# Kernel optimization log

Measured on AMD Instinct MI355X. Metric: run time of the kernel, lower is better.

Reference implementation:

```python
import jax, jax.numpy as jnp
import numpy as np

I3 = jnp.eye(3, dtype=jnp.float32)
G_VEC = jnp.array([0.0, 0.0, -9.80665], dtype=jnp.float32)
# Q diag: [cov_omega x3, cov_acc x3, cov_b_omega x3, cov_b_acc x3, cov_Rot_c_i x3, cov_t_c_i x3]
Q_DIAG = jnp.array([1e-3] * 3 + [1e-2] * 3 + [6e-9] * 3 + [2e-4] * 3 + [1e-9] * 3 + [1e-9] * 3, dtype=jnp.float32)
N_NORM_ROT = 100
N_NORM_ROT_CI = 1000


def skew(v):
    z = jnp.zeros_like(v[0])
    return jnp.stack([jnp.stack([z, -v[2], v[1]]),
                      jnp.stack([v[2], z, -v[0]]),
                      jnp.stack([-v[1], v[0], z])])


def so3exp(phi):
    a2 = jnp.sum(phi * phi)
    small = a2 < 1e-12
    a = jnp.sqrt(jnp.where(small, 1.0, a2))
    axis = phi / a
    c, s = jnp.cos(a), jnp.sin(a)
    big = c * I3 + (1.0 - c) * jnp.outer(axis, axis) + s * skew(axis)
    return jnp.where(small, I3 + skew(phi), big)


def sen3exp(xi):
    # SE_2(3) exponential: xi[:3]=rotation, xi[3:9]=(v, p) parts
    phi = xi[:3]
    a2 = jnp.sum(phi * phi)
    small = a2 < 1e-12
    a = jnp.sqrt(jnp.where(small, 1.0, a2))
    axis = phi / a
    c, s = jnp.cos(a), jnp.sin(a)
    sk = skew(axis)
    R = jnp.where(small, I3 + skew(phi),
                  c * I3 + (1.0 - c) * jnp.outer(axis, axis) + s * sk)
    J = jnp.where(small, I3 + 0.5 * skew(phi),
                  (s / a) * I3 + (1.0 - s / a) * jnp.outer(axis, axis) + ((1.0 - c) / a) * sk)
    x = J @ xi[3:].reshape(2, 3).T  # (3,2): columns are dv, dp
    return R, x


def normalize_rot(R):
    # Polar-factor re-orthonormalization (equivalent to the SVD-based
    # normalize_rot for near-rotation matrices), via Newton-Schulz iteration
    # which is smooth and jit/vjp friendly.
    def body(X, _):
        return 1.5 * X - 0.5 * (X @ X.T @ X), None
    X, _ = jax.lax.scan(body, R, None, length=8)
    return X


def from_rpy(roll, pitch, yaw):
    cr, sr = jnp.cos(roll), jnp.sin(roll)
    cp, sp = jnp.cos(pitch), jnp.sin(pitch)
    cy, sy = jnp.cos(yaw), jnp.sin(yaw)
    one = jnp.ones_like(cr)
    zero = jnp.zeros_like(cr)
    Rx = jnp.stack([jnp.stack([one, zero, zero]), jnp.stack([zero, cr, -sr]), jnp.stack([zero, sr, cr])])
    Ry = jnp.stack([jnp.stack([cp, zero, sp]), jnp.stack([zero, one, zero]), jnp.stack([-sp, zero, cp])])
    Rz = jnp.stack([jnp.stack([cy, -sy, zero]), jnp.stack([sy, cy, zero]), jnp.stack([zero, zero, one])])
    return Rz @ Ry @ Rx


def init_covariance():
    P = jnp.zeros((21, 21), dtype=jnp.float32)
    P = P.at[:2, :2].set(1e-3 * jnp.eye(2))     # cov_Rot0 (no yaw error)
    P = P.at[3:5, 3:5].set(0.1 * jnp.eye(2))    # cov_v0
    P = P.at[9:12, 9:12].set(6e-3 * I3)         # cov_b_omega0
    P = P.at[12:15, 12:15].set(4e-3 * I3)       # cov_b_acc0
    P = P.at[15:18, 15:18].set(1e-6 * I3)       # cov_Rot_c_i0
    P = P.at[18:21, 18:21].set(5e-3 * I3)       # cov_t_c_i0
    return P


def propagate_cov(P, Rot, v, p, dt):
    F = jnp.zeros((21, 21), dtype=P.dtype)
    F = F.at[3:6, :3].set(skew(G_VEC))
    F = F.at[6:9, 3:6].set(I3)
    F = F.at[:3, 9:12].set(-Rot)
    F = F.at[3:6, 9:12].set(-skew(v) @ Rot)
    F = F.at[3:6, 12:15].set(-Rot)
    F = F.at[6:9, 9:12].set(-skew(p) @ Rot)
    G = jnp.zeros((21, 18), dtype=P.dtype)
    G = G.at[:3, :3].set(Rot)
    G = G.at[3:6, 3:6].set(Rot)
    G = G.at[9:12, 6:9].set(I3)
    G = G.at[12:15, 9:12].set(I3)
    G = G.at[15:18, 12:15].set(I3)
    G = G.at[18:21, 15:18].set(I3)
    F = F * dt
    G = G * dt
    F2 = F @ F
    Phi = jnp.eye(21, dtype=P.dtype) + F + 0.5 * F2 + (F2 @ F) / 6.0  # 3rd-order expm
    return Phi @ (P + (G * Q_DIAG[None, :]) @ G.T) @ Phi.T


def _step(carry, xs):
    Rot, v, p, b_om, b_ac, Rci, tci, P = carry
    u_i, dt_i, mcov_i, i = xs
    # ---- propagate ----
    acc = Rot @ (u_i[3:6] - b_ac) + G_VEC
    v_n = v + acc * dt_i
    p_n = p + v * dt_i + 0.5 * acc * dt_i * dt_i
    Rot_n = Rot @ so3exp((u_i[:3] - b_om) * dt_i)
    P_n = propagate_cov(P, Rot, v, p, dt_i)
    # ---- update: zero lateral/vertical body-velocity pseudo-measurement ----
    omega = u_i[:3] - b_om
    Rot_body = Rot_n @ Rci
    v_imu = Rot_n.T @ v_n
    v_body = Rci.T @ v_imu + skew(tci) @ omega
    H = jnp.zeros((2, 21), dtype=P.dtype)
    H = H.at[:, 3:6].set(Rot_body.T[1:])
    H = H.at[:, 15:18].set((Rci.T @ skew(v_imu))[1:])
    H = H.at[:, 9:12].set(skew(tci)[1:])
    H = H.at[:, 18:21].set(-skew(omega)[1:])
    r = -v_body[1:]
    Rm = jnp.diag(mcov_i)
    S = H @ P_n @ H.T + Rm                    # (2,2)
    K = jnp.linalg.solve(S, H @ P_n).T        # K = P H^T S^-1 (P, S symmetric)
    dx = K @ r                                 # (21,)
    dR, dxi = sen3exp(dx[:9])
    Rot_u = dR @ Rot_n
    v_u = dR @ v_n + dxi[:, 0]
    p_u = dR @ p_n + dxi[:, 1]
    b_om_u = b_om + dx[9:12]
    b_ac_u = b_ac + dx[12:15]
    Rci_u = so3exp(dx[15:18]) @ Rci
    tci_u = tci + dx[18:21]
    IKH = jnp.eye(21, dtype=P.dtype) - K @ H
    P_u = IKH @ P_n @ IKH.T + K @ Rm @ K.T    # Joseph form
    P_u = 0.5 * (P_u + P_u.T)
    Rot_u = jnp.where(i % N_NORM_ROT == 0, normalize_rot(Rot_u), Rot_u)
    Rci_u = jnp.where(i % N_NORM_ROT_CI == 0, normalize_rot(Rci_u), Rci_u)
    carry = (Rot_u, v_u, p_u, b_om_u, b_ac_u, Rci_u, tci_u, P_u)
    return carry, (Rot_u, v_u, p_u, b_om_u, b_ac_u, Rci_u, tci_u)


def _forward(t, u, measurements_covs, v_mes, p_mes, ang0, N):
    dt = t[1:N] - t[:N - 1]
    Rot0 = from_rpy(ang0[0], ang0[1], ang0[2])
    z3 = jnp.zeros(3, dtype=u.dtype)
    carry0 = (Rot0, v_mes[0], z3, z3, z3, I3, z3, init_covariance())
    xs = (u[1:N], dt, measurements_covs[1:N], jnp.arange(1, N))
    _, ys = jax.lax.scan(_step, carry0, xs)
    Rot = jnp.concatenate([Rot0[None], ys[0]], axis=0)
    v = jnp.concatenate([v_mes[0][None], ys[1]], axis=0)
    p = jnp.concatenate([z3[None], ys[2]], axis=0)
    b_omega = jnp.concatenate([z3[None], ys[3]], axis=0)
    b_acc = jnp.concatenate([z3[None], ys[4]], axis=0)
    Rot_c_i = jnp.concatenate([I3[None], ys[5]], axis=0)
    t_c_i = jnp.concatenate([z3[None], ys[6]], axis=0)
    return (Rot, v, p, b_omega, b_acc, Rot_c_i, t_c_i)


def setup_inputs() -> dict:
    key = jax.random.key(0)
    N = 20000  # 200 s at 100 Hz IMU
    k0, k1, k2, k3, k4, k5 = jax.random.split(key, 6)
    t = jnp.arange(N, dtype=jnp.float32) * 0.01
    gyro = 0.01 * jax.random.normal(k0, (N, 3), dtype=jnp.float32)
    acc = jnp.array([0.0, 0.0, 9.80665], jnp.float32) + 0.1 * jax.random.normal(k1, (N, 3), dtype=jnp.float32)
    u = jnp.concatenate([gyro, acc], axis=1)
    measurements_covs = 0.1 + jax.random.uniform(k2, (N, 2), dtype=jnp.float32)
    v_mes = jax.random.normal(k3, (N, 3), dtype=jnp.float32)
    p_mes = jax.random.normal(k4, (N, 3), dtype=jnp.float32)
    ang0 = 0.01 * jax.random.normal(k5, (3,), dtype=jnp.float32)
    return dict(t=t, u=u, measurements_covs=measurements_covs, v_mes=v_mes, p_mes=p_mes, ang0=ang0, N=N)


def reference(t, u, measurements_covs, v_mes, p_mes, ang0, N):
    return _forward(t, u, measurements_covs, v_mes, p_mes, ang0, N)
```

## Files before the change

### kernel.cpp

```cpp
#include <hip/hip_runtime.h>

#define GRAV 9.80665f
#define WAVE_SYNC() do { \
    asm volatile("s_waitcnt lgkmcnt(0)" ::: "memory"); \
    __builtin_amdgcn_sched_barrier(0); \
  } while(0)

__device__ __forceinline__ float sel3(int r, float a0, float a1, float a2){
  float x = (r==1)? a1 : a0;
  return (r>=2)? a2 : x;
}
__device__ __forceinline__ float pick12(int k, const float* H){
  float s=H[0];
  s=(k==1)?H[1]:s; s=(k==2)?H[2]:s; s=(k==3)?H[3]:s; s=(k==4)?H[4]:s;
  s=(k==5)?H[5]:s; s=(k==6)?H[6]:s; s=(k==7)?H[7]:s; s=(k==8)?H[8]:s;
  s=(k==9)?H[9]:s; s=(k==10)?H[10]:s; s=(k==11)?H[11]:s;
  return s;
}
__device__ __forceinline__ float pick9(int k, const float* X){
  float s=X[0];
  s=(k==1)?X[1]:s; s=(k==2)?X[2]:s; s=(k==3)?X[3]:s; s=(k==4)?X[4]:s;
  s=(k==5)?X[5]:s; s=(k==6)?X[6]:s; s=(k==7)?X[7]:s; s=(k==8)?X[8]:s;
  return s;
}

__device__ __forceinline__ void mm33(float* __restrict__ O, const float* A, const float* B){
#pragma unroll
  for(int r=0;r<3;++r){
#pragma unroll
    for(int c=0;c<3;++c){
      O[r*3+c] = A[r*3+0]*B[0*3+c] + A[r*3+1]*B[1*3+c] + A[r*3+2]*B[2*3+c];
    }
  }
}

__device__ __forceinline__ void rot_from_t2(float t_, float p0, float p1, float p2, float* R){
  float c_, k1_, k2_;
  if (t_ < 1e-4f){
    c_  = 1.f - t_*(0.5f - t_*((1.f/24.f) - t_*(1.f/720.f)));
    k2_ = 1.f - t_*((1.f/6.f) - t_*((1.f/120.f) - t_*(1.f/5040.f)));
    k1_ = 0.5f - t_*((1.f/24.f) - t_*(1.f/720.f));
  } else {
    float a = sqrtf(t_);
    c_ = __cosf(a);
    float s = __sinf(a);
    k2_ = s/a;
    k1_ = (1.f - c_)/t_;
  }
  R[0]=c_+k1_*p0*p0;      R[1]=k1_*p0*p1-k2_*p2;  R[2]=k1_*p0*p2+k2_*p1;
  R[3]=k1_*p0*p1+k2_*p2;  R[4]=c_+k1_*p1*p1;      R[5]=k1_*p1*p2-k2_*p0;
  R[6]=k1_*p0*p2-k2_*p1;  R[7]=k1_*p1*p2+k2_*p0;  R[8]=c_+k1_*p2*p2;
}

__device__ __forceinline__ void normalize_rot9(float* X){
#pragma unroll 1
  for(int it=0; it<8; ++it){
    float Y[9], Z[9];
#pragma unroll
    for(int r=0;r<3;++r)
#pragma unroll
      for(int c=0;c<3;++c)
        Y[r*3+c] = X[r*3+0]*X[c*3+0] + X[r*3+1]*X[c*3+1] + X[r*3+2]*X[c*3+2];
#pragma unroll
    for(int r=0;r<3;++r)
#pragma unroll
      for(int c=0;c<3;++c)
        Z[r*3+c] = Y[r*3+0]*X[0*3+c] + Y[r*3+1]*X[1*3+c] + Y[r*3+2]*X[2*3+c];
#pragma unroll
    for(int e=0;e<9;++e) X[e] = 1.5f*X[e] - 0.5f*Z[e];
  }
}

__device__ __forceinline__ float pick_state(int l,
    const float* Rt, const float* vv, const float* pp,
    const float* bw, const float* ba, const float* Rc, const float* tc){
  float s = Rt[0];
  s=(l==1)?Rt[1]:s;  s=(l==2)?Rt[2]:s;  s=(l==3)?Rt[3]:s;  s=(l==4)?Rt[4]:s;
  s=(l==5)?Rt[5]:s;  s=(l==6)?Rt[6]:s;  s=(l==7)?Rt[7]:s;  s=(l==8)?Rt[8]:s;
  s=(l==9)?vv[0]:s;  s=(l==10)?vv[1]:s; s=(l==11)?vv[2]:s;
  s=(l==12)?pp[0]:s; s=(l==13)?pp[1]:s; s=(l==14)?pp[2]:s;
  s=(l==15)?bw[0]:s; s=(l==16)?bw[1]:s; s=(l==17)?bw[2]:s;
  s=(l==18)?ba[0]:s; s=(l==19)?ba[1]:s; s=(l==20)?ba[2]:s;
  s=(l==21)?Rc[0]:s; s=(l==22)?Rc[1]:s; s=(l==23)?Rc[2]:s;
  s=(l==24)?Rc[3]:s; s=(l==25)?Rc[4]:s; s=(l==26)?Rc[5]:s;
  s=(l==27)?Rc[6]:s; s=(l==28)?Rc[7]:s; s=(l==29)?Rc[8]:s;
  s=(l==30)?tc[0]:s; s=(l==31)?tc[1]:s; s=(l==32)?tc[2]:s;
  return s;
}

__global__ __launch_bounds__(128,1)
void iekf_scan_kernel(const float* __restrict__ t,
                      const float* __restrict__ u,
                      const float* __restrict__ mcov,
                      const float* __restrict__ v_mes,
                      const float* __restrict__ ang0,
                      float* __restrict__ out, int N)
{
  const int tid = threadIdx.x;
  const bool isA = (tid < 64);
  const int l = tid & 63;

  __shared__ float  Pm[441];
  __shared__ float  Eb[441];
  __shared__ float  PnS[441];
  __shared__ float2 HPs2[21];
  __shared__ __align__(16) float stS[36];
  __shared__ __align__(16) float Hds[24];

  for (int e=tid; e<441; e+=128){
    int r=e/21, c=e-(e/21)*21;
    float vI=0.f;
    if (r==c){
      if (r<2) vI=0.001f;
      else if (r==3||r==4) vI=0.1f;
      else if (r>=9&&r<12) vI=0.006f;
      else if (r>=12&&r<15) vI=0.004f;
      else if (r>=15&&r<18) vI=1e-6f;
      else if (r>=18) vI=0.005f;
    }
    Pm[e]=vI;
  }

  int ostr=0; float* op = out;
  {
    int obase=0, ooff=0;
    if (l<9)       {obase=0;    ostr=9; ooff=l;}
    else if (l<12) {obase=9*N;  ostr=3; ooff=l-9;}
    else if (l<15) {obase=12*N; ostr=3; ooff=l-12;}
    else if (l<18) {obase=15*N; ostr=3; ooff=l-15;}
    else if (l<21) {obase=18*N; ostr=3; ooff=l-18;}
    else if (l<30) {obase=21*N; ostr=9; ooff=l-21;}
    else           {obase=30*N; ostr=3; ooff=l-30;}
    op = out + obase + ooff;
  }

  const int g21 = l/21;
  const int c21 = l - g21*21;
  const int cw  = 9 + 4*g21;
  int l1 = l+21; if (l1>=63) l1-=63;
  int l2 = l+42; if (l2>=63) l2-=63;
  static const int cols[12] = {3,4,5, 9,10,11, 15,16,17, 18,19,20};

  float tA=0.f, tB=0.f, cu[6]={0,0,0,0,0,0}, cm0=0.f, cm1=0.f;

  if (isA){
    float Rt0[9], vv0[3], pp0[3], bw0a[3], ba0a[3], Rc0[9], tc0a[3];
    {
      float rl = ang0[0], pt = ang0[1], yw = ang0[2];
      float cr=cosf(rl), sr=sinf(rl), cp=cosf(pt), sp=sinf(pt), cy=cosf(yw), sy=sinf(yw);
      Rt0[0]=cy*cp; Rt0[1]=cy*sp*sr - sy*cr; Rt0[2]=cy*sp*cr + sy*sr;
      Rt0[3]=sy*cp; Rt0[4]=sy*sp*sr + cy*cr; Rt0[5]=sy*sp*cr - cy*sr;
      Rt0[6]=-sp;   Rt0[7]=cp*sr;            Rt0[8]=cp*cr;
    }
    vv0[0]=v_mes[0]; vv0[1]=v_mes[1]; vv0[2]=v_mes[2];
#pragma unroll
    for(int k=0;k<3;++k){ pp0[k]=0.f; bw0a[k]=0.f; ba0a[k]=0.f; tc0a[k]=0.f; }
    Rc0[0]=1.f;Rc0[1]=0.f;Rc0[2]=0.f;Rc0[3]=0.f;Rc0[4]=1.f;Rc0[5]=0.f;Rc0[6]=0.f;Rc0[7]=0.f;Rc0[8]=1.f;

    float sv = pick_state(l, Rt0, vv0, pp0, bw0a, ba0a, Rc0, tc0a);
    if (l<33){ op[0] = sv; stS[l] = sv; }

    tA = t[0]; tB = t[1];
#pragma unroll
    for(int k=0;k<6;++k) cu[k]=u[6+k];
    cm0 = mcov[2]; cm1 = mcov[3];
    if (l>=33 && l<36) stS[l] = sel3(l-33, tB-tA, cm0, cm1);
  }
  __syncthreads();

  int nx100=100, nx1000=1000;

#pragma unroll 1
  for (int i=1; i<N; ++i){
    float Rn[9]; float vn0=0,vn1=0,vn2=0, pn0=0,pn1=0,pn2=0;
    float H0[12], H1[12];
    float rr0=0, rr1=0, crm0=0, crm1=0;
    float bw0=0,bw1=0,bw2=0, ba0=0,ba1=0,ba2=0, tc0=0,tc1=0,tc2=0;
    float Rc[9];
    float Bs0=0,Bs1=0,Bs2=0,Cs0=0,Cs1=0,Cs2=0,Ds0=0,Ds1=0,Ds2=0;
    float dt=0, gdt=0, hdt=0;
    float pnv[7]; float hpr0=0, hpr1=0;
#pragma unroll
    for(int k=0;k<7;++k) pnv[k]=0.f;
#pragma unroll
    for(int k=0;k<9;++k){ Rn[k]=0.f; Rc[k]=0.f; }
#pragma unroll
    for(int k=0;k<12;++k){ H0[k]=0.f; H1[k]=0.f; }

    if (isA){
      dt = tB - tA;
      float u0=cu[0], u1=cu[1], u2=cu[2], u3=cu[3], u4=cu[4], u5=cu[5];
      crm0=cm0; crm1=cm1;
      if (i+1 < N){
        tA = tB; tB = t[i+1];
#pragma unroll
        for(int k=0;k<6;++k) cu[k]=u[(i+1)*6+k];
        cm0 = mcov[(i+1)*2]; cm1 = mcov[(i+1)*2+1];
      }
      const float4* st4 = (const float4*)stS;
      float4 q0=st4[0], q1=st4[1], q2=st4[2], q3=st4[3], q4=st4[4], q5=st4[5], q6=st4[6], q7=st4[7], q8=st4[8];
      float Rt[9] = {q0.x,q0.y,q0.z,q0.w,q1.x,q1.y,q1.z,q1.w,q2.x};
      float vv0s=q2.y, vv1s=q2.z, vv2s=q2.w;
      float pp0s=q3.x, pp1s=q3.y, pp2s=q3.z;
      bw0=q3.w; bw1=q4.x; bw2=q4.y;
      ba0=q4.z; ba1=q4.w; ba2=q5.x;
      Rc[0]=q5.y; Rc[1]=q5.z; Rc[2]=q5.w; Rc[3]=q6.x; Rc[4]=q6.y; Rc[5]=q6.z;
      Rc[6]=q6.w; Rc[7]=q7.x; Rc[8]=q7.y;
      tc0=q7.z; tc1=q7.w; tc2=q8.x;

      float hdt2 = 0.5f*dt*dt;
      float w0=u0-bw0, w1=u1-bw1, w2=u2-bw2;
      float aa0=u3-ba0, aa1=u4-ba1, aa2=u5-ba2;
      float acc0 = Rt[0]*aa0+Rt[1]*aa1+Rt[2]*aa2;
      float acc1 = Rt[3]*aa0+Rt[4]*aa1+Rt[5]*aa2;
      float acc2 = Rt[6]*aa0+Rt[7]*aa1+Rt[8]*aa2 - GRAV;
      vn0=vv0s+acc0*dt; vn1=vv1s+acc1*dt; vn2=vv2s+acc2*dt;
      pn0=pp0s+vv0s*dt+acc0*hdt2;
      pn1=pp1s+vv1s*dt+acc1*hdt2;
      pn2=pp2s+vv2s*dt+acc2*hdt2;
      float ph0=w0*dt, ph1=w1*dt, ph2=w2*dt;
      float dRs[9]; rot_from_t2(ph0*ph0+ph1*ph1+ph2*ph2, ph0,ph1,ph2, dRs);
      mm33(Rn, Rt, dRs);
      float Rb[9]; mm33(Rb, Rn, Rc);
      float vi0 = Rn[0]*vn0+Rn[3]*vn1+Rn[6]*vn2;
      float vi1 = Rn[1]*vn0+Rn[4]*vn1+Rn[7]*vn2;
      float vi2 = Rn[2]*vn0+Rn[5]*vn1+Rn[8]*vn2;
      float vb1 = Rc[1]*vi0+Rc[4]*vi1+Rc[7]*vi2 + (tc2*w0 - tc0*w2);
      float vb2 = Rc[2]*vi0+Rc[5]*vi1+Rc[8]*vi2 + (tc0*w1 - tc1*w0);
      rr0 = -vb1; rr1 = -vb2;

      H0[0]=Rb[1]; H0[1]=Rb[4]; H0[2]=Rb[7];
      H1[0]=Rb[2]; H1[1]=Rb[5]; H1[2]=Rb[8];
      H0[3]=tc2;  H0[4]=0.f;  H0[5]=-tc0;
      H1[3]=-tc1; H1[4]=tc0;  H1[5]=0.f;
      H0[6]=Rc[4]*vi2 - Rc[7]*vi1;  H0[7]=Rc[7]*vi0 - Rc[1]*vi2;  H0[8]=Rc[1]*vi1 - Rc[4]*vi0;
      H1[6]=Rc[5]*vi2 - Rc[8]*vi1;  H1[7]=Rc[8]*vi0 - Rc[2]*vi2;  H1[8]=Rc[2]*vi1 - Rc[5]*vi0;
      H0[9]=-w2; H0[10]=0.f; H0[11]=w0;
      H1[9]=w1;  H1[10]=-w0; H1[11]=0.f;

      if (l<24){
        float hv = (l<12)? pick12(l,H0) : pick12(l-12,H1);
        Hds[l] = hv;
      }
    } else {
      const float4* st4 = (const float4*)stS;
      float4 q0=st4[0], q1=st4[1], q2=st4[2], q3=st4[3], q8=st4[8];
      float Rt[9] = {q0.x,q0.y,q0.z,q0.w,q1.x,q1.y,q1.z,q1.w,q2.x};
      float vv0s=q2.y, vv1s=q2.z, vv2s=q2.w;
      float pp0s=q3.x, pp1s=q3.y, pp2s=q3.z;
      dt = q8.y; crm0 = q8.z; crm1 = q8.w;
      float dt2=dt*dt; gdt=GRAV*dt; hdt=0.5f*dt;
      float g6=gdt*dt*(1.0f/6.0f);

      float Bm[9], Cab[9], D2a[9];
#pragma unroll
      for(int k=0;k<3;++k){
        float b0=-dt*Rt[k], b1=-dt*Rt[3+k], b2=-dt*Rt[6+k];
        float c0=dt*(vv2s*Rt[3+k]-vv1s*Rt[6+k]);
        float c1=dt*(vv0s*Rt[6+k]-vv2s*Rt[k]);
        float c2=dt*(vv1s*Rt[k]-vv0s*Rt[3+k]);
        float d0=dt*(pp2s*Rt[3+k]-pp1s*Rt[6+k]);
        float d1=dt*(pp0s*Rt[6+k]-pp2s*Rt[k]);
        float d2=dt*(pp1s*Rt[k]-pp0s*Rt[3+k]);
        Bm[k]=b0; Bm[3+k]=b1; Bm[6+k]=b2;
        Cab[k]=c0+0.5f*gdt*b1; Cab[3+k]=c1-0.5f*gdt*b0; Cab[6+k]=c2;
        D2a[k]=d0+hdt*c0+g6*b1; D2a[3+k]=d1+hdt*c1-g6*b0; D2a[6+k]=d2+hdt*c2;
      }
      Bs0=sel3(g21,Bm[0],Bm[3],Bm[6]);  Bs1=sel3(g21,Bm[1],Bm[4],Bm[7]);  Bs2=sel3(g21,Bm[2],Bm[5],Bm[8]);
      Cs0=sel3(g21,Cab[0],Cab[3],Cab[6]);Cs1=sel3(g21,Cab[1],Cab[4],Cab[7]);Cs2=sel3(g21,Cab[2],Cab[5],Cab[8]);
      Ds0=sel3(g21,D2a[0],D2a[3],D2a[6]);Ds1=sel3(g21,D2a[1],D2a[4],D2a[7]);Ds2=sel3(g21,D2a[2],D2a[5],D2a[8]);

      float RRT00=Rt[0]*Rt[0]+Rt[1]*Rt[1]+Rt[2]*Rt[2];
      float RRT01=Rt[0]*Rt[3]+Rt[1]*Rt[4]+Rt[2]*Rt[5];
      float RRT02=Rt[0]*Rt[6]+Rt[1]*Rt[7]+Rt[2]*Rt[8];
      float RRT11=Rt[3]*Rt[3]+Rt[4]*Rt[4]+Rt[5]*Rt[5];
      float RRT12=Rt[3]*Rt[6]+Rt[4]*Rt[7]+Rt[5]*Rt[8];
      float RRT22=Rt[6]*Rt[6]+Rt[7]*Rt[7]+Rt[8]*Rt[8];
      float q0d=0.001f*dt2, q1d=0.01f*dt2;
      float q69=6e-9f*dt2, q24=2e-4f*dt2, q19=1e-9f*dt2;

      if (l<63){
        int c = c21;
        bool cl3 = (c<3);
        bool c36 = (c>=3 && c<6);
        float R0c  = sel3(c,   RRT00, RRT01, RRT02);
        float R1c  = sel3(c,   RRT01, RRT11, RRT12);
        float R2c  = sel3(c,   RRT02, RRT12, RRT22);
        float R0c3 = sel3(c-3, RRT00, RRT01, RRT02);
        float R1c3 = sel3(c-3, RRT01, RRT11, RRT12);
        float R2c3 = sel3(c-3, RRT02, RRT12, RRT22);
        float d0  = cl3 ? q0d*R0c : 0.f;
        float d1  = cl3 ? q0d*R1c : 0.f;
        float dg  = cl3 ? q0d*sel3(g21,R0c,R1c,R2c) : 0.f;
        float dg3 = c36 ? q1d*sel3(g21,R0c3,R1c3,R2c3) : 0.f;

        float m0  = Pm[c]            + d0;
        float m1  = Pm[21+c]         + d1;
        float mr  = Pm[g21*21+c]     + dg;
        float m3r = Pm[(3+g21)*21+c] + dg3;
        float m6r = Pm[(6+g21)*21+c];
        float m9  = Pm[9*21+c]  + ((c==9) ? q69 : 0.f);
        float m10 = Pm[10*21+c] + ((c==10)? q69 : 0.f);
        float m11 = Pm[11*21+c] + ((c==11)? q69 : 0.f);
        float m12 = Pm[12*21+c] + ((c==12)? q24 : 0.f);
        float m13 = Pm[13*21+c] + ((c==13)? q24 : 0.f);
        float m14 = Pm[14*21+c] + ((c==14)? q24 : 0.f);

        float Ar = (g21==0)? gdt*m1 : (g21==1)? -gdt*m0 : 0.f;
        float bterm = Bs0*m12+Bs1*m13+Bs2*m14;
        float e0 = mr + Bs0*m9+Bs1*m10+Bs2*m11;
        float e1 = m3r + Ar + Cs0*m9+Cs1*m10+Cs2*m11 + bterm;
        float e2 = m6r + hdt*Ar + dt*m3r + Ds0*m9+Ds1*m10+Ds2*m11 + hdt*bterm;
        Eb[g21*21+c]=e0; Eb[(3+g21)*21+c]=e1; Eb[(6+g21)*21+c]=e2;
#pragma unroll
        for (int jj=0;jj<4;++jj){
          int row = cw+jj;
          float qd = (row<12)? q69 : (row<15)? q24 : q19;
          Eb[row*21+c] = Pm[row*21+c] + ((row==c)? qd : 0.f);
        }
      }
    }
    __syncthreads();

    if (!isA){
      const float4* h4p = (const float4*)Hds;
      float4 h0v=h4p[0], h1v=h4p[1], h2v=h4p[2], h3v=h4p[3], h4v=h4p[4], h5v=h4p[5];
      H0[0]=h0v.x; H0[1]=h0v.y; H0[2]=h0v.z; H0[3]=h0v.w;
      H0[4]=h1v.x; H0[5]=h1v.y; H0[6]=h1v.z; H0[7]=h1v.w;
      H0[8]=h2v.x; H0[9]=h2v.y; H0[10]=h2v.z; H0[11]=h2v.w;
      H1[0]=h3v.x; H1[1]=h3v.y; H1[2]=h3v.z; H1[3]=h3v.w;
      H1[4]=h4v.x; H1[5]=h4v.y; H1[6]=h4v.z; H1[7]=h4v.w;
      H1[8]=h5v.x; H1[9]=h5v.y; H1[10]=h5v.z; H1[11]=h5v.w;

      float p0=0.f, p1=0.f;
      if (l<63){
        int r = c21;
        const float* Er = Eb + r*21;
        float e0a=Er[0], e1a=Er[1];
        float eg=Er[g21], e3g=Er[3+g21], e6g=Er[6+g21];
        float e9=Er[9],e10=Er[10],e11=Er[11],e12=Er[12],e13=Er[13],e14=Er[14];
        float Ag = (g21==0)? gdt*e1a : (g21==1)? -gdt*e0a : 0.f;
        float bterm = Bs0*e12+Bs1*e13+Bs2*e14;
        pnv[0] = eg + Bs0*e9+Bs1*e10+Bs2*e11;
        pnv[1] = e3g + Ag + Cs0*e9+Cs1*e10+Cs2*e11 + bterm;
        pnv[2] = e6g + hdt*Ag + dt*e3g + Ds0*e9+Ds1*e10+Ds2*e11 + hdt*bterm;
        pnv[3] = Er[cw]; pnv[4] = Er[cw+1]; pnv[5] = Er[cw+2]; pnv[6] = Er[cw+3];

        PnS[r*21 + g21]   = pnv[0];
        PnS[r*21 + 3+g21] = pnv[1];
        PnS[r*21 + 6+g21] = pnv[2];
        PnS[r*21 + cw]    = pnv[3];
        PnS[r*21 + cw+1]  = pnv[4];
        PnS[r*21 + cw+2]  = pnv[5];
        PnS[r*21 + cw+3]  = pnv[6];

        float c1a = sel3(g21, H0[0], H0[1], H0[2]);
        float c3a = sel3(g21, H0[3], 0.f,   H0[8]);
        float c4a = sel3(g21, H0[4], 0.f,   H0[9]);
        float c5a = sel3(g21, H0[5], H0[6], H0[10]);
        float c6a = sel3(g21, 0.f,   H0[7], H0[11]);
        float c1b = sel3(g21, H1[0], H1[1], H1[2]);
        float c3b = sel3(g21, H1[3], 0.f,   H1[8]);
        float c4b = sel3(g21, H1[4], 0.f,   H1[9]);
        float c5b = sel3(g21, H1[5], H1[6], H1[10]);
        float c6b = sel3(g21, 0.f,   H1[7], H1[11]);
        p0 = c1a*pnv[1] + c3a*pnv[3] + c4a*pnv[4] + c5a*pnv[5] + c6a*pnv[6];
        p1 = c1b*pnv[1] + c3b*pnv[3] + c4b*pnv[4] + c5b*pnv[5] + c6b*pnv[6];
      }
      hpr0 = p0 + __shfl(p0, l1) + __shfl(p0, l2);
      hpr1 = p1 + __shfl(p1, l1) + __shfl(p1, l2);
      if (l<21) HPs2[l] = make_float2(hpr0, hpr1);
    }
    __syncthreads();

    if (isA){
      float2 myhp = HPs2[(l<21)? l : 0];
      float hph00=0.f, hph01=0.f, hph10=0.f, hph11=0.f;
#pragma unroll
      for(int k=0;k<12;++k){
        float2 hp = HPs2[cols[k]];
        hph00 += hp.x*H0[k]; hph01 += hp.x*H1[k];
        hph10 += hp.y*H0[k]; hph11 += hp.y*H1[k];
      }
      float s00 = hph00 + crm0, s01 = hph01, s10 = hph10, s11 = hph11 + crm1;
      float idet = 1.0f/(s00*s11 - s01*s10);
      float i00 =  s11*idet, i01 = -s01*idet, i10 = -s10*idet, i11 = s00*idet;
      float K0 = i00*myhp.x + i01*myhp.y;
      float K1 = i10*myhp.x + i11*myhp.y;
      float dxval = K0*rr0 + K1*rr1;

      int db = __float_as_int(dxval);
      float dx0 = __int_as_float(__builtin_amdgcn_readlane(db, 0));
      float dx1 = __int_as_float(__builtin_amdgcn_readlane(db, 1));
      float dx2 = __int_as_float(__builtin_amdgcn_readlane(db, 2));
      float dx3 = __int_as_float(__builtin_amdgcn_readlane(db, 3));
      float dx4 = __int_as_float(__builtin_amdgcn_readlane(db, 4));
      float dx5 = __int_as_float(__builtin_amdgcn_readlane(db, 5));
      float dx6 = __int_as_float(__builtin_amdgcn_readlane(db, 6));
      float dx7 = __int_as_float(__builtin_amdgcn_readlane(db, 7));
      float dx8 = __int_as_float(__builtin_amdgcn_readlane(db, 8));
      float dx15 = __int_as_float(__builtin_amdgcn_readlane(db, 15));
      float dx16 = __int_as_float(__builtin_amdgcn_readlane(db, 16));
      float dx17 = __int_as_float(__builtin_amdgcn_readlane(db, 17));
      int src = (l>=30 && l<33)? (l-12) : ((l>=15 && l<21)? (l-6) : 0);
      float dxadd = __shfl(dxval, src);

      float t2x = dx0*dx0+dx1*dx1+dx2*dx2;
      float cX,k1X,k2X,j1X;
      if (t2x < 1e-4f){
        cX  = 1.f - t2x*(0.5f - t2x*((1.f/24.f) - t2x*(1.f/720.f)));
        k2X = 1.f - t2x*((1.f/6.f) - t2x*((1.f/120.f) - t2x*(1.f/5040.f)));
        k1X = 0.5f - t2x*((1.f/24.f) - t2x*(1.f/720.f));
        j1X = (1.f/6.f) - t2x*((1.f/120.f) - t2x*(1.f/5040.f));
      } else {
        float a = sqrtf(t2x);
        cX = __cosf(a);
        float s = __sinf(a);
        k2X = s/a; k1X = (1.f-cX)/t2x; j1X = (1.f-k2X)/t2x;
      }
      float dR[9];
      dR[0]=cX+k1X*dx0*dx0;      dR[1]=k1X*dx0*dx1-k2X*dx2; dR[2]=k1X*dx0*dx2+k2X*dx1;
      dR[3]=k1X*dx0*dx1+k2X*dx2; dR[4]=cX+k1X*dx1*dx1;      dR[5]=k1X*dx1*dx2-k2X*dx0;
      dR[6]=k1X*dx0*dx2-k2X*dx1; dR[7]=k1X*dx1*dx2+k2X*dx0; dR[8]=cX+k1X*dx2*dx2;
      float Jm[9];
      Jm[0]=k2X+j1X*dx0*dx0;      Jm[1]=j1X*dx0*dx1-k1X*dx2; Jm[2]=j1X*dx0*dx2+k1X*dx1;
      Jm[3]=j1X*dx0*dx1+k1X*dx2;  Jm[4]=k2X+j1X*dx1*dx1;     Jm[5]=j1X*dx1*dx2-k1X*dx0;
      Jm[6]=j1X*dx0*dx2-k1X*dx1;  Jm[7]=j1X*dx1*dx2+k1X*dx0; Jm[8]=k2X+j1X*dx2*dx2;
      float Ec[9];
      rot_from_t2(dx15*dx15+dx16*dx16+dx17*dx17, dx15,dx16,dx17, Ec);

      float myval = 0.f;
      if (l<9){
        int ro=(l>=6)?2:((l>=3)?1:0); int co=l-3*ro;
        float d0=sel3(ro,dR[0],dR[3],dR[6]), d1=sel3(ro,dR[1],dR[4],dR[7]), d2=sel3(ro,dR[2],dR[5],dR[8]);
        float n0=sel3(co,Rn[0],Rn[1],Rn[2]), n1=sel3(co,Rn[3],Rn[4],Rn[5]), n2=sel3(co,Rn[6],Rn[7],Rn[8]);
        myval = d0*n0 + d1*n1 + d2*n2;
      } else if (l<15){
        int j=l-9; bool isv=(j<3); int ro = isv? j : (j-3);
        float x0 = isv? vn0:pn0, x1 = isv? vn1:pn1, x2 = isv? vn2:pn2;
        float y0 = isv? dx3:dx6, y1 = isv? dx4:dx7, y2 = isv? dx5:dx8;
        float d0=sel3(ro,dR[0],dR[3],dR[6]), d1=sel3(ro,dR[1],dR[4],dR[7]), d2=sel3(ro,dR[2],dR[5],dR[8]);
        float j0=sel3(ro,Jm[0],Jm[3],Jm[6]), j1m=sel3(ro,Jm[1],Jm[4],Jm[7]), j2m=sel3(ro,Jm[2],Jm[5],Jm[8]);
        myval = d0*x0 + d1*x1 + d2*x2 + j0*y0 + j1m*y1 + j2m*y2;
      } else if (l<21){
        float old = (l<18)? sel3(l-15,bw0,bw1,bw2) : sel3(l-18,ba0,ba1,ba2);
        myval = old + dxadd;
      } else if (l<30){
        int j=l-21; int ro=(j>=6)?2:((j>=3)?1:0); int co=j-3*ro;
        float e0=sel3(ro,Ec[0],Ec[3],Ec[6]), e1=sel3(ro,Ec[1],Ec[4],Ec[7]), e2=sel3(ro,Ec[2],Ec[5],Ec[8]);
        float r0=sel3(co,Rc[0],Rc[1],Rc[2]), r1=sel3(co,Rc[3],Rc[4],Rc[5]), r2=sel3(co,Rc[6],Rc[7],Rc[8]);
        myval = e0*r0 + e1*r1 + e2*r2;
      } else if (l<33){
        myval = sel3(l-30,tc0,tc1,tc2) + dxadd;
      }
      if (l<33) stS[l] = myval;
      if (l>=33 && l<36) stS[l] = sel3(l-33, tB-tA, cm0, cm1);

      bool n100 = (i==nx100), n1000 = (i==nx1000);
      if (n100) nx100 += 100;
      if (n1000) nx1000 += 1000;
      if (n100 || n1000){
        WAVE_SYNC();
        if (n100){
          float X[9];
#pragma unroll
          for (int k=0;k<9;++k) X[k]=stS[k];
          normalize_rot9(X);
          if (l<9){ myval = pick9(l,X); stS[l] = myval; }
        }
        if (n1000){
          float Y[9];
#pragma unroll
          for (int k=0;k<9;++k) Y[k]=stS[21+k];
          normalize_rot9(Y);
          if (l>=21 && l<30){ myval = pick9(l-21,Y); stS[l] = myval; }
        }
      }
      if (l<33) op[i*ostr] = myval;
    } else {
      float hph00=0.f, hph01=0.f, hph10=0.f, hph11=0.f;
#pragma unroll
      for(int k=0;k<12;++k){
        float2 hp = HPs2[cols[k]];
        hph00 += hp.x*H0[k]; hph01 += hp.x*H1[k];
        hph10 += hp.y*H0[k]; hph11 += hp.y*H1[k];
      }
      float s00 = hph00 + crm0, s01 = hph01, s10 = hph10, s11 = hph11 + crm1;
      float idet = 1.0f/(s00*s11 - s01*s10);
      float i00 =  s11*idet, i01 = -s01*idet, i10 = -s10*idet, i11 = s00*idet;
      float s01q = 0.5f*(s01 + s10);
      float K0 = i00*hpr0 + i01*hpr1;
      float K1 = i10*hpr0 + i11*hpr1;

      if (l<63){
        int r = c21;
#pragma unroll
        for (int s=0;s<7;++s){
          int j = (s<3)? (g21 + 3*s) : (cw + (s-3));
          float pnT = PnS[j*21 + r];
          float2 hpj = HPs2[j];
          float kjx = i00*hpj.x + i01*hpj.y;
          float kjy = i10*hpj.x + i11*hpj.y;
          float base  = 0.5f*(pnv[s] + pnT);
          float cross = (K0*hpj.x + K1*hpj.y) + (kjx*hpr0 + kjy*hpr1);
          float quad  = (K0*kjx)*s00 + (K0*kjy + K1*kjx)*s01q + (K1*kjy)*s11;
          Pm[r*21+j] = base - cross + quad;
        }
      }
    }
    __syncthreads();
  }
}

extern "C" void kernel_launch(void* const* d_in, const int* in_sizes, int n_in,
                              void* d_out, int out_size, void* d_ws, size_t ws_size,
                              hipStream_t stream) {
  (void)n_in; (void)out_size; (void)d_ws; (void)ws_size;
  const float* t     = (const float*)d_in[0];
  const float* u     = (const float*)d_in[1];
  const float* mcov  = (const float*)d_in[2];
  const float* v_mes = (const float*)d_in[3];
  const float* ang0  = (const float*)d_in[5];
  int N = in_sizes[0];
  iekf_scan_kernel<<<dim3(1), dim3(128), 0, stream>>>(t, u, mcov, v_mes, ang0, (float*)d_out, N);
}
```

Measured before the change: 51.56 ms.

## Merge two specialized waves into a single wavefront with intra-wave syncs

Collapses the 128-thread two-wave kernel, where one wave did the state update and the other the covariance propagation, into one 64-lane wavefront. Every step now runs state and covariance work in sequence, replacing __syncthreads barriers with lightweight LDS waitcnt syncs and readlane broadcasts of the HP vector. The aim is to cut per-step workgroup barrier latency in this serial scan, at the cost of losing the overlap between the two waves' independent work.

```diff
diff --git a/kernel.cpp b/kernel.cpp
--- a/kernel.cpp
+++ b/kernel.cpp
@@ -10,12 +10,8 @@
   float x = (r==1)? a1 : a0;
   return (r>=2)? a2 : x;
 }
-__device__ __forceinline__ float pick12(int k, const float* H){
-  float s=H[0];
-  s=(k==1)?H[1]:s; s=(k==2)?H[2]:s; s=(k==3)?H[3]:s; s=(k==4)?H[4]:s;
-  s=(k==5)?H[5]:s; s=(k==6)?H[6]:s; s=(k==7)?H[7]:s; s=(k==8)?H[8]:s;
-  s=(k==9)?H[9]:s; s=(k==10)?H[10]:s; s=(k==11)?H[11]:s;
-  return s;
+__device__ __forceinline__ float RL(float v, int k){
+  return __int_as_float(__builtin_amdgcn_readlane(__float_as_int(v), k));
 }
 __device__ __forceinline__ float pick9(int k, const float* X){
   float s=X[0];
@@ -88,7 +84,7 @@
   return s;
 }
 
-__global__ __launch_bounds__(128,1)
+__global__ __launch_bounds__(64,1)
 void iekf_scan_kernel(const float* __restrict__ t,
                       const float* __restrict__ u,
                       const float* __restrict__ mcov,
@@ -96,18 +92,14 @@
                       const float* __restrict__ ang0,
                       float* __restrict__ out, int N)
 {
-  const int tid = threadIdx.x;
-  const bool isA = (tid < 64);
-  const int l = tid & 63;
-
+  const int l = threadIdx.x;
   __shared__ float  Pm[441];
   __shared__ float  Eb[441];
   __shared__ float  PnS[441];
   __shared__ float2 HPs2[21];
   __shared__ __align__(16) float stS[36];
-  __shared__ __align__(16) float Hds[24];
-
-  for (int e=tid; e<441; e+=128){
+
+  for (int e=l; e<441; e+=64){
     int r=e/21, c=e-(e/21)*21;
     float vI=0.f;
     if (r==c){
@@ -141,374 +133,325 @@
   int l2 = l+42; if (l2>=63) l2-=63;
   static const int cols[12] = {3,4,5, 9,10,11, 15,16,17, 18,19,20};
 
-  float tA=0.f, tB=0.f, cu[6]={0,0,0,0,0,0}, cm0=0.f, cm1=0.f;
-
-  if (isA){
-    float Rt0[9], vv0[3], pp0[3], bw0a[3], ba0a[3], Rc0[9], tc0a[3];
-    {
-      float rl = ang0[0], pt = ang0[1], yw = ang0[2];
-      float cr=cosf(rl), sr=sinf(rl), cp=cosf(pt), sp=sinf(pt), cy=cosf(yw), sy=sinf(yw);
-      Rt0[0]=cy*cp; Rt0[1]=cy*sp*sr - sy*cr; Rt0[2]=cy*sp*cr + sy*sr;
-      Rt0[3]=sy*cp; Rt0[4]=sy*sp*sr + cy*cr; Rt0[5]=sy*sp*cr - cy*sr;
-      Rt0[6]=-sp;   Rt0[7]=cp*sr;            Rt0[8]=cp*cr;
-    }
+  {
+    float Rt0[9], vv0[3], pp0[3], bwa[3], baa[3], Rc0[9], tca[3];
+    float rl = ang0[0], pt = ang0[1], yw = ang0[2];
+    float cr=cosf(rl), sr=sinf(rl), cp=cosf(pt), sp=sinf(pt), cy=cosf(yw), sy=sinf(yw);
+    Rt0[0]=cy*cp; Rt0[1]=cy*sp*sr - sy*cr; Rt0[2]=cy*sp*cr + sy*sr;
+    Rt0[3]=sy*cp; Rt0[4]=sy*sp*sr + cy*cr; Rt0[5]=sy*sp*cr - cy*sr;
+    Rt0[6]=-sp;   Rt0[7]=cp*sr;            Rt0[8]=cp*cr;
     vv0[0]=v_mes[0]; vv0[1]=v_mes[1]; vv0[2]=v_mes[2];
 #pragma unroll
-    for(int k=0;k<3;++k){ pp0[k]=0.f; bw0a[k]=0.f; ba0a[k]=0.f; tc0a[k]=0.f; }
+    for(int k=0;k<3;++k){ pp0[k]=0.f; bwa[k]=0.f; baa[k]=0.f; tca[k]=0.f; }
     Rc0[0]=1.f;Rc0[1]=0.f;Rc0[2]=0.f;Rc0[3]=0.f;Rc0[4]=1.f;Rc0[5]=0.f;Rc0[6]=0.f;Rc0[7]=0.f;Rc0[8]=1.f;
-
-    float sv = pick_state(l, Rt0, vv0, pp0, bw0a, ba0a, Rc0, tc0a);
+    float sv = pick_state(l, Rt0, vv0, pp0, bwa, baa, Rc0, tca);
     if (l<33){ op[0] = sv; stS[l] = sv; }
-
-    tA = t[0]; tB = t[1];
-#pragma unroll
-    for(int k=0;k<6;++k) cu[k]=u[6+k];
-    cm0 = mcov[2]; cm1 = mcov[3];
-    if (l>=33 && l<36) stS[l] = sel3(l-33, tB-tA, cm0, cm1);
-  }
-  __syncthreads();
+    if (l>=33 && l<36) stS[l] = 0.f;
+  }
+  WAVE_SYNC();
+
+  float tA = t[0], tB = t[1];
+  float cu[6];
+#pragma unroll
+  for(int k=0;k<6;++k) cu[k]=u[6+k];
+  float cm0=mcov[2], cm1=mcov[3];
 
   int nx100=100, nx1000=1000;
 
 #pragma unroll 1
   for (int i=1; i<N; ++i){
-    float Rn[9]; float vn0=0,vn1=0,vn2=0, pn0=0,pn1=0,pn2=0;
+    float dt = tB - tA;
+    float u0=cu[0], u1=cu[1], u2=cu[2], u3=cu[3], u4=cu[4], u5=cu[5];
+    float crm0=cm0, crm1=cm1;
+    if (i+1 < N){
+      tA = tB; tB = t[i+1];
+#pragma unroll
+      for(int k=0;k<6;++k) cu[k]=u[(i+1)*6+k];
+      cm0 = mcov[(i+1)*2]; cm1 = mcov[(i+1)*2+1];
+    }
+
+    const float4* st4 = (const float4*)stS;
+    float4 q0=st4[0], q1=st4[1], q2=st4[2], q3=st4[3], q4=st4[4], q5=st4[5], q6=st4[6], q7=st4[7], q8=st4[8];
+    float Rt[9] = {q0.x,q0.y,q0.z,q0.w,q1.x,q1.y,q1.z,q1.w,q2.x};
+    float vv0s=q2.y, vv1s=q2.z, vv2s=q2.w;
+    float pp0s=q3.x, pp1s=q3.y, pp2s=q3.z;
+    float bw0=q3.w, bw1=q4.x, bw2=q4.y;
+    float ba0=q4.z, ba1=q4.w, ba2=q5.x;
+    float Rc[9] = {q5.y,q5.z,q5.w,q6.x,q6.y,q6.z,q6.w,q7.x,q7.y};
+    float tc0=q7.z, tc1=q7.w, tc2=q8.x;
+
+    float dt2=dt*dt, gdt=GRAV*dt, hdt=0.5f*dt, hdt2=0.5f*dt*dt;
+    float hgdt2 = 0.5f*gdt*dt;
+    float g6d   = gdt*dt2*(1.0f/6.0f);
+
+    float w0=u0-bw0, w1=u1-bw1, w2=u2-bw2;
+    float aa0=u3-ba0, aa1=u4-ba1, aa2=u5-ba2;
+    float acc0 = Rt[0]*aa0+Rt[1]*aa1+Rt[2]*aa2;
+    float acc1 = Rt[3]*aa0+Rt[4]*aa1+Rt[5]*aa2;
+    float acc2 = Rt[6]*aa0+Rt[7]*aa1+Rt[8]*aa2 - GRAV;
+    float vn0=vv0s+acc0*dt, vn1=vv1s+acc1*dt, vn2=vv2s+acc2*dt;
+    float pn0=pp0s+vv0s*dt+acc0*hdt2;
+    float pn1=pp1s+vv1s*dt+acc1*hdt2;
+    float pn2=pp2s+vv2s*dt+acc2*hdt2;
+    float ph0=w0*dt, ph1=w1*dt, ph2=w2*dt;
+    float dRs[9]; rot_from_t2(ph0*ph0+ph1*ph1+ph2*ph2, ph0,ph1,ph2, dRs);
+    float Rn[9]; mm33(Rn, Rt, dRs);
+
+    float RtG[3], RtA[3], RtB[3];
+#pragma unroll
+    for(int k=0;k<3;++k){
+      float r0=Rt[k], r3=Rt[3+k], r6=Rt[6+k];
+      RtG[k] = sel3(g21, r0, r3, r6);
+      RtA[k] = sel3(g21, r3, r6, r0);
+      RtB[k] = sel3(g21, r6, r0, r3);
+    }
+    float vAs = sel3(g21, vv2s, vv0s, vv1s), vBs = sel3(g21, vv1s, vv2s, vv0s);
+    float pAs = sel3(g21, pp2s, pp0s, pp1s), pBs = sel3(g21, pp1s, pp2s, pp0s);
+    float Bs0,Bs1,Bs2, Cs0,Cs1,Cs2, Ds0,Ds1,Ds2;
+    {
+      float bs[3], cs[3], ds[3];
+#pragma unroll
+      for(int k=0;k<3;++k){
+        bs[k] = -dt*RtG[k];
+        float craw = dt*(vAs*RtA[k] - vBs*RtB[k]);
+        float selC = sel3(g21, -RtA[k], RtB[k], 0.f);
+        cs[k] = craw + hgdt2*selC;
+        float draw = dt*(pAs*RtA[k] - pBs*RtB[k]);
+        ds[k] = draw + hdt*craw + g6d*selC;
+      }
+      Bs0=bs[0];Bs1=bs[1];Bs2=bs[2];
+      Cs0=cs[0];Cs1=cs[1];Cs2=cs[2];
+      Ds0=ds[0];Ds1=ds[1];Ds2=ds[2];
+    }
+
+    float q0d=0.001f*dt2, q1d=0.01f*dt2;
+    float q69=6e-9f*dt2, q24=2e-4f*dt2, q19=1e-9f*dt2;
+
+    if (l<63){
+      int c = c21;
+      bool cl3 = (c<3);
+      bool c36 = (c>=3 && c<6);
+      int csel = c36 ? (c-3) : (cl3 ? c : 0);
+      float Rtc0 = sel3(csel, Rt[0], Rt[3], Rt[6]);
+      float Rtc1 = sel3(csel, Rt[1], Rt[4], Rt[7]);
+      float Rtc2 = sel3(csel, Rt[2], Rt[5], Rt[8]);
+      float dot0 = Rt[0]*Rtc0 + Rt[1]*Rtc1 + Rt[2]*Rtc2;
+      float dot1 = Rt[3]*Rtc0 + Rt[4]*Rtc1 + Rt[5]*Rtc2;
+      float dotg = RtG[0]*Rtc0 + RtG[1]*Rtc1 + RtG[2]*Rtc2;
+      float d0  = cl3 ? q0d*dot0 : 0.f;
+      float d1  = cl3 ? q0d*dot1 : 0.f;
+      float dg  = cl3 ? q0d*dotg : 0.f;
+      float dg3 = c36 ? q1d*dotg : 0.f;
+
+      float m0  = Pm[c]            + d0;
+      float m1  = Pm[21+c]         + d1;
+      float mr  = Pm[g21*21+c]     + dg;
+      float m3r = Pm[(3+g21)*21+c] + dg3;
+      float m6r = Pm[(6+g21)*21+c];
+      float m9  = Pm[9*21+c]  + ((c==9) ? q69 : 0.f);
+      float m10 = Pm[10*21+c] + ((c==10)? q69 : 0.f);
+      float m11 = Pm[11*21+c] + ((c==11)? q69 : 0.f);
+      float m12 = Pm[12*21+c] + ((c==12)? q24 : 0.f);
+      float m13 = Pm[13*21+c] + ((c==13)? q24 : 0.f);
+      float m14 = Pm[14*21+c] + ((c==14)? q24 : 0.f);
+
+      float Ar = (g21==0)? gdt*m1 : (g21==1)? -gdt*m0 : 0.f;
+      float bterm = Bs0*m12+Bs1*m13+Bs2*m14;
+      float e0 = mr + Bs0*m9+Bs1*m10+Bs2*m11;
+      float e1 = m3r + Ar + Cs0*m9+Cs1*m10+Cs2*m11 + bterm;
+      float e2 = m6r + hdt*Ar + dt*m3r + Ds0*m9+Ds1*m10+Ds2*m11 + hdt*bterm;
+      Eb[g21*21+c]=e0; Eb[(3+g21)*21+c]=e1; Eb[(6+g21)*21+c]=e2;
+#pragma unroll
+      for (int jj=0;jj<4;++jj){
+        int row = cw+jj;
+        float qd = (row<12)? q69 : (row<15)? q24 : q19;
+        Eb[row*21+c] = Pm[row*21+c] + ((row==c)? qd : 0.f);
+      }
+    }
+
     float H0[12], H1[12];
-    float rr0=0, rr1=0, crm0=0, crm1=0;
-    float bw0=0,bw1=0,bw2=0, ba0=0,ba1=0,ba2=0, tc0=0,tc1=0,tc2=0;
-    float Rc[9];
-    float Bs0=0,Bs1=0,Bs2=0,Cs0=0,Cs1=0,Cs2=0,Ds0=0,Ds1=0,Ds2=0;
-    float dt=0, gdt=0, hdt=0;
-    float pnv[7]; float hpr0=0, hpr1=0;
-#pragma unroll
-    for(int k=0;k<7;++k) pnv[k]=0.f;
-#pragma unroll
-    for(int k=0;k<9;++k){ Rn[k]=0.f; Rc[k]=0.f; }
-#pragma unroll
-    for(int k=0;k<12;++k){ H0[k]=0.f; H1[k]=0.f; }
-
-    if (isA){
-      dt = tB - tA;
-      float u0=cu[0], u1=cu[1], u2=cu[2], u3=cu[3], u4=cu[4], u5=cu[5];
-      crm0=cm0; crm1=cm1;
-      if (i+1 < N){
-        tA = tB; tB = t[i+1];
-#pragma unroll
-        for(int k=0;k<6;++k) cu[k]=u[(i+1)*6+k];
-        cm0 = mcov[(i+1)*2]; cm1 = mcov[(i+1)*2+1];
-      }
-      const float4* st4 = (const float4*)stS;
-      float4 q0=st4[0], q1=st4[1], q2=st4[2], q3=st4[3], q4=st4[4], q5=st4[5], q6=st4[6], q7=st4[7], q8=st4[8];
-      float Rt[9] = {q0.x,q0.y,q0.z,q0.w,q1.x,q1.y,q1.z,q1.w,q2.x};
-      float vv0s=q2.y, vv1s=q2.z, vv2s=q2.w;
-      float pp0s=q3.x, pp1s=q3.y, pp2s=q3.z;
-      bw0=q3.w; bw1=q4.x; bw2=q4.y;
-      ba0=q4.z; ba1=q4.w; ba2=q5.x;
-      Rc[0]=q5.y; Rc[1]=q5.z; Rc[2]=q5.w; Rc[3]=q6.x; Rc[4]=q6.y; Rc[5]=q6.z;
-      Rc[6]=q6.w; Rc[7]=q7.x; Rc[8]=q7.y;
-      tc0=q7.z; tc1=q7.w; tc2=q8.x;
-
-      float hdt2 = 0.5f*dt*dt;
-      float w0=u0-bw0, w1=u1-bw1, w2=u2-bw2;
-      float aa0=u3-ba0, aa1=u4-ba1, aa2=u5-ba2;
-      float acc0 = Rt[0]*aa0+Rt[1]*aa1+Rt[2]*aa2;
-      float acc1 = Rt[3]*aa0+Rt[4]*aa1+Rt[5]*aa2;
-      float acc2 = Rt[6]*aa0+Rt[7]*aa1+Rt[8]*aa2 - GRAV;
-      vn0=vv0s+acc0*dt; vn1=vv1s+acc1*dt; vn2=vv2s+acc2*dt;
-      pn0=pp0s+vv0s*dt+acc0*hdt2;
-      pn1=pp1s+vv1s*dt+acc1*hdt2;
-      pn2=pp2s+vv2s*dt+acc2*hdt2;
-      float ph0=w0*dt, ph1=w1*dt, ph2=w2*dt;
-      float dRs[9]; rot_from_t2(ph0*ph0+ph1*ph1+ph2*ph2, ph0,ph1,ph2, dRs);
-      mm33(Rn, Rt, dRs);
-      float Rb[9]; mm33(Rb, Rn, Rc);
-      float vi0 = Rn[0]*vn0+Rn[3]*vn1+Rn[6]*vn2;
-      float vi1 = Rn[1]*vn0+Rn[4]*vn1+Rn[7]*vn2;
-      float vi2 = Rn[2]*vn0+Rn[5]*vn1+Rn[8]*vn2;
+    float vi0, vi1, vi2, rr0, rr1;
+    {
+      float Rb1 = Rn[0]*Rc[1]+Rn[1]*Rc[4]+Rn[2]*Rc[7];
+      float Rb4 = Rn[3]*Rc[1]+Rn[4]*Rc[4]+Rn[5]*Rc[7];
+      float Rb7 = Rn[6]*Rc[1]+Rn[7]*Rc[4]+Rn[8]*Rc[7];
+      float Rb2 = Rn[0]*Rc[2]+Rn[1]*Rc[5]+Rn[2]*Rc[8];
+      float Rb5 = Rn[3]*Rc[2]+Rn[4]*Rc[5]+Rn[5]*Rc[8];
+      float Rb8 = Rn[6]*Rc[2]+Rn[7]*Rc[5]+Rn[8]*Rc[8];
+      vi0 = Rn[0]*vn0+Rn[3]*vn1+Rn[6]*vn2;
+      vi1 = Rn[1]*vn0+Rn[4]*vn1+Rn[7]*vn2;
+      vi2 = Rn[2]*vn0+Rn[5]*vn1+Rn[8]*vn2;
       float vb1 = Rc[1]*vi0+Rc[4]*vi1+Rc[7]*vi2 + (tc2*w0 - tc0*w2);
       float vb2 = Rc[2]*vi0+Rc[5]*vi1+Rc[8]*vi2 + (tc0*w1 - tc1*w0);
       rr0 = -vb1; rr1 = -vb2;
-
-      H0[0]=Rb[1]; H0[1]=Rb[4]; H0[2]=Rb[7];
-      H1[0]=Rb[2]; H1[1]=Rb[5]; H1[2]=Rb[8];
+      H0[0]=Rb1; H0[1]=Rb4; H0[2]=Rb7;
+      H1[0]=Rb2; H1[1]=Rb5; H1[2]=Rb8;
       H0[3]=tc2;  H0[4]=0.f;  H0[5]=-tc0;
       H1[3]=-tc1; H1[4]=tc0;  H1[5]=0.f;
       H0[6]=Rc[4]*vi2 - Rc[7]*vi1;  H0[7]=Rc[7]*vi0 - Rc[1]*vi2;  H0[8]=Rc[1]*vi1 - Rc[4]*vi0;
       H1[6]=Rc[5]*vi2 - Rc[8]*vi1;  H1[7]=Rc[8]*vi0 - Rc[2]*vi2;  H1[8]=Rc[2]*vi1 - Rc[5]*vi0;
       H0[9]=-w2; H0[10]=0.f; H0[11]=w0;
       H1[9]=w1;  H1[10]=-w0; H1[11]=0.f;
-
-      if (l<24){
-        float hv = (l<12)? pick12(l,H0) : pick12(l-12,H1);
-        Hds[l] = hv;
+    }
+    WAVE_SYNC();
+
+    float pnv[7];
+#pragma unroll
+    for(int k=0;k<7;++k) pnv[k]=0.f;
+    float p0=0.f, p1=0.f;
+    if (l<63){
+      int r = c21;
+      const float* Er = Eb + r*21;
+      float e0a=Er[0], e1a=Er[1];
+      float eg=Er[g21], e3g=Er[3+g21], e6g=Er[6+g21];
+      float e9=Er[9],e10=Er[10],e11=Er[11],e12=Er[12],e13=Er[13],e14=Er[14];
+      float Ag = (g21==0)? gdt*e1a : (g21==1)? -gdt*e0a : 0.f;
+      float bterm = Bs0*e12+Bs1*e13+Bs2*e14;
+      pnv[0] = eg + Bs0*e9+Bs1*e10+Bs2*e11;
+      pnv[1] = e3g + Ag + Cs0*e9+Cs1*e10+Cs2*e11 + bterm;
+      pnv[2] = e6g + hdt*Ag + dt*e3g + Ds0*e9+Ds1*e10+Ds2*e11 + hdt*bterm;
+      pnv[3] = Er[cw]; pnv[4] = Er[cw+1]; pnv[5] = Er[cw+2]; pnv[6] = Er[cw+3];
+
+      PnS[r*21 + g21]   = pnv[0];
+      PnS[r*21 + 3+g21] = pnv[1];
+      PnS[r*21 + 6+g21] = pnv[2];
+      PnS[r*21 + cw]    = pnv[3];
+      PnS[r*21 + cw+1]  = pnv[4];
+      PnS[r*21 + cw+2]  = pnv[5];
+      PnS[r*21 + cw+3]  = pnv[6];
+
+      float c1a = sel3(g21, H0[0], H0[1], H0[2]);
+      float c3a = sel3(g21, H0[3], 0.f,   H0[8]);
+      float c4a = sel3(g21, H0[4], 0.f,   H0[9]);
+      float c5a = sel3(g21, H0[5], H0[6], H0[10]);
+      float c6a = sel3(g21, 0.f,   H0[7], H0[11]);
+      float c1b = sel3(g21, H1[0], H1[1], H1[2]);
+      float c3b = sel3(g21, H1[3], 0.f,   H1[8]);
+      float c4b = sel3(g21, H1[4], 0.f,   H1[9]);
+      float c5b = sel3(g21, H1[5], H1[6], H1[10]);
+      float c6b = sel3(g21, 0.f,   H1[7], H1[11]);
+      p0 = c1a*pnv[1] + c3a*pnv[3] + c4a*pnv[4] + c5a*pnv[5] + c6a*pnv[6];
+      p1 = c1b*pnv[1] + c3b*pnv[3] + c4b*pnv[4] + c5b*pnv[5] + c6b*pnv[6];
+    }
+    float hpr0 = p0 + __shfl(p0, l1) + __shfl(p0, l2);
+    float hpr1 = p1 + __shfl(p1, l1) + __shfl(p1, l2);
+    if (l<21) HPs2[l] = make_float2(hpr0, hpr1);
+
+    float hph00=0.f, hph01=0.f, hph10=0.f, hph11=0.f;
+#pragma unroll
+    for(int k=0;k<12;++k){
+      float hp0 = RL(hpr0, cols[k]);
+      float hp1 = RL(hpr1, cols[k]);
+      hph00 += hp0*H0[k]; hph01 += hp0*H1[k];
+      hph10 += hp1*H0[k]; hph11 += hp1*H1[k];
+    }
+    float s00 = hph00 + crm0, s01 = hph01, s10 = hph10, s11 = hph11 + crm1;
+    float idet = 1.0f/(s00*s11 - s01*s10);
+    float i00 =  s11*idet, i01 = -s01*idet, i10 = -s10*idet, i11 = s00*idet;
+    float K0 = i00*hpr0 + i01*hpr1;
+    float K1 = i10*hpr0 + i11*hpr1;
+    float s01q = 0.5f*(s01 + s10);
+    float dxval = K0*rr0 + K1*rr1;
+
+    float dx0 = RL(dxval,0), dx1 = RL(dxval,1), dx2 = RL(dxval,2);
+    float dx3 = RL(dxval,3), dx4 = RL(dxval,4), dx5 = RL(dxval,5);
+    float dx6 = RL(dxval,6), dx7 = RL(dxval,7), dx8 = RL(dxval,8);
+    float dx15 = RL(dxval,15), dx16 = RL(dxval,16), dx17 = RL(dxval,17);
+    int src = (l>=30 && l<33)? (l-12) : ((l>=15 && l<21)? (l-6) : 0);
+    float dxadd = __shfl(dxval, src);
+
+    float t2x = dx0*dx0+dx1*dx1+dx2*dx2;
+    float cX,k1X,k2X,j1X;
+    if (t2x < 1e-4f){
+      cX  = 1.f - t2x*(0.5f - t2x*((1.f/24.f) - t2x*(1.f/720.f)));
+      k2X = 1.f - t2x*((1.f/6.f) - t2x*((1.f/120.f) - t2x*(1.f/5040.f)));
+      k1X = 0.5f - t2x*((1.f/24.f) - t2x*(1.f/720.f));
+      j1X = (1.f/6.f) - t2x*((1.f/120.f) - t2x*(1.f/5040.f));
+    } else {
+      float a = sqrtf(t2x);
+      cX = __cosf(a);
+      float s = __sinf(a);
+      k2X = s/a; k1X = (1.f-cX)/t2x; j1X = (1.f-k2X)/t2x;
+    }
+    float dR[9];
+    dR[0]=cX+k1X*dx0*dx0;      dR[1]=k1X*dx0*dx1-k2X*dx2; dR[2]=k1X*dx0*dx2+k2X*dx1;
+    dR[3]=k1X*dx0*dx1+k2X*dx2; dR[4]=cX+k1X*dx1*dx1;      dR[5]=k1X*dx1*dx2-k2X*dx0;
+    dR[6]=k1X*dx0*dx2-k2X*dx1; dR[7]=k1X*dx1*dx2+k2X*dx0; dR[8]=cX+k1X*dx2*dx2;
+    float Jm[9];
+    Jm[0]=k2X+j1X*dx0*dx0;      Jm[1]=j1X*dx0*dx1-k1X*dx2; Jm[2]=j1X*dx0*dx2+k1X*dx1;
+    Jm[3]=j1X*dx0*dx1+k1X*dx2;  Jm[4]=k2X+j1X*dx1*dx1;     Jm[5]=j1X*dx1*dx2-k1X*dx0;
+    Jm[6]=j1X*dx0*dx2-k1X*dx1;  Jm[7]=j1X*dx1*dx2+k1X*dx0; Jm[8]=k2X+j1X*dx2*dx2;
+    float Ec[9];
+    rot_from_t2(dx15*dx15+dx16*dx16+dx17*dx17, dx15,dx16,dx17, Ec);
+
+    WAVE_SYNC();
+
+    if (l<63){
+      int r = c21;
+#pragma unroll
+      for (int s=0;s<7;++s){
+        int j = (s<3)? (g21 + 3*s) : (cw + (s-3));
+        float pnT = PnS[j*21 + r];
+        float2 hpj = HPs2[j];
+        float kjx = i00*hpj.x + i01*hpj.y;
+        float kjy = i10*hpj.x + i11*hpj.y;
+        float base  = 0.5f*(pnv[s] + pnT);
+        float cross = (K0*hpj.x + K1*hpj.y) + (kjx*hpr0 + kjy*hpr1);
+        float quad  = (K0*kjx)*s00 + (K0*kjy + K1*kjx)*s01q + (K1*kjy)*s11;
+        Pm[r*21+j] = base - cross + quad;
       }
-    } else {
-      const float4* st4 = (const float4*)stS;
-      float4 q0=st4[0], q1=st4[1], q2=st4[2], q3=st4[3], q8=st4[8];
-      float Rt[9] = {q0.x,q0.y,q0.z,q0.w,q1.x,q1.y,q1.z,q1.w,q2.x};
-      float vv0s=q2.y, vv1s=q2.z, vv2s=q2.w;
-      float pp0s=q3.x, pp1s=q3.y, pp2s=q3.z;
-      dt = q8.y; crm0 = q8.z; crm1 = q8.w;
-      float dt2=dt*dt; gdt=GRAV*dt; hdt=0.5f*dt;
-      float g6=gdt*dt*(1.0f/6.0f);
-
-      float Bm[9], Cab[9], D2a[9];
-#pragma unroll
-      for(int k=0;k<3;++k){
-        float b0=-dt*Rt[k], b1=-dt*Rt[3+k], b2=-dt*Rt[6+k];
-        float c0=dt*(vv2s*Rt[3+k]-vv1s*Rt[6+k]);
-        float c1=dt*(vv0s*Rt[6+k]-vv2s*Rt[k]);
-        float c2=dt*(vv1s*Rt[k]-vv0s*Rt[3+k]);
-        float d0=dt*(pp2s*Rt[3+k]-pp1s*Rt[6+k]);
-        float d1=dt*(pp0s*Rt[6+k]-pp2s*Rt[k]);
-        float d2=dt*(pp1s*Rt[k]-pp0s*Rt[3+k]);
-        Bm[k]=b0; Bm[3+k]=b1; Bm[6+k]=b2;
-        Cab[k]=c0+0.5f*gdt*b1; Cab[3+k]=c1-0.5f*gdt*b0; Cab[6+k]=c2;
-        D2a[k]=d0+hdt*c0+g6*b1; D2a[3+k]=d1+hdt*c1-g6*b0; D2a[6+k]=d2+hdt*c2;
+    }
+
+    float myval = 0.f;
+    if (l<9){
+      int ro=(l>=6)?2:((l>=3)?1:0); int co=l-3*ro;
+      float d0=sel3(ro,dR[0],dR[3],dR[6]), d1=sel3(ro,dR[1],dR[4],dR[7]), d2=sel3(ro,dR[2],dR[5],dR[8]);
+      float n0=sel3(co,Rn[0],Rn[1],Rn[2]), n1=sel3(co,Rn[3],Rn[4],Rn[5]), n2=sel3(co,Rn[6],Rn[7],Rn[8]);
+      myval = d0*n0 + d1*n1 + d2*n2;
+    } else if (l<15){
+      int j=l-9; bool isv=(j<3); int ro = isv? j : (j-3);
+      float x0 = isv? vn0:pn0, x1 = isv? vn1:pn1, x2 = isv? vn2:pn2;
+      float y0 = isv? dx3:dx6, y1 = isv? dx4:dx7, y2 = isv? dx5:dx8;
+      float d0=sel3(ro,dR[0],dR[3],dR[6]), d1=sel3(ro,dR[1],dR[4],dR[7]), d2=sel3(ro,dR[2],dR[5],dR[8]);
+      float j0=sel3(ro,Jm[0],Jm[3],Jm[6]), j1m=sel3(ro,Jm[1],Jm[4],Jm[7]), j2m=sel3(ro,Jm[2],Jm[5],Jm[8]);
+      myval = d0*x0 + d1*x1 + d2*x2 + j0*y0 + j1m*y1 + j2m*y2;
+    } else if (l<21){
+      float old = (l<18)? sel3(l-15,bw0,bw1,bw2) : sel3(l-18,ba0,ba1,ba2);
+      myval = old + dxadd;
+    } else if (l<30){
+      int j=l-21; int ro=(j>=6)?2:((j>=3)?1:0); int co=j-3*ro;
+      float e0=sel3(ro,Ec[0],Ec[3],Ec[6]), e1=sel3(ro,Ec[1],Ec[4],Ec[7]), e2=sel3(ro,Ec[2],Ec[5],Ec[8]);
+      float r0=sel3(co,Rc[0],Rc[1],Rc[2]), r1=sel3(co,Rc[3],Rc[4],Rc[5]), r2=sel3(co,Rc[6],Rc[7],Rc[8]);
+      myval = e0*r0 + e1*r1 + e2*r2;
+    } else if (l<33){
+      myval = sel3(l-30,tc0,tc1,tc2) + dxadd;
+    }
+    if (l<33) stS[l] = myval;
+
+    bool n100 = (i==nx100), n1000 = (i==nx1000);
+    if (n100) nx100 += 100;
+    if (n1000) nx1000 += 1000;
+    if (n100 || n1000){
+      WAVE_SYNC();
+      if (n100){
+        float X[9];
+#pragma unroll
+        for (int k=0;k<9;++k) X[k]=stS[k];
+        normalize_rot9(X);
+        if (l<9){ myval = pick9(l,X); stS[l] = myval; }
       }
-      Bs0=sel3(g21,Bm[0],Bm[3],Bm[6]);  Bs1=sel3(g21,Bm[1],Bm[4],Bm[7]);  Bs2=sel3(g21,Bm[2],Bm[5],Bm[8]);
-      Cs0=sel3(g21,Cab[0],Cab[3],Cab[6]);Cs1=sel3(g21,Cab[1],Cab[4],Cab[7]);Cs2=sel3(g21,Cab[2],Cab[5],Cab[8]);
-      Ds0=sel3(g21,D2a[0],D2a[3],D2a[6]);Ds1=sel3(g21,D2a[1],D2a[4],D2a[7]);Ds2=sel3(g21,D2a[2],D2a[5],D2a[8]);
-
-      float RRT00=Rt[0]*Rt[0]+Rt[1]*Rt[1]+Rt[2]*Rt[2];
-      float RRT01=Rt[0]*Rt[3]+Rt[1]*Rt[4]+Rt[2]*Rt[5];
-      float RRT02=Rt[0]*Rt[6]+Rt[1]*Rt[7]+Rt[2]*Rt[8];
-      float RRT11=Rt[3]*Rt[3]+Rt[4]*Rt[4]+Rt[5]*Rt[5];
-      float RRT12=Rt[3]*Rt[6]+Rt[4]*Rt[7]+Rt[5]*Rt[8];
-      float RRT22=Rt[6]*Rt[6]+Rt[7]*Rt[7]+Rt[8]*Rt[8];
-      float q0d=0.001f*dt2, q1d=0.01f*dt2;
-      float q69=6e-9f*dt2, q24=2e-4f*dt2, q19=1e-9f*dt2;
-
-      if (l<63){
-        int c = c21;
-        bool cl3 = (c<3);
-        bool c36 = (c>=3 && c<6);
-        float R0c  = sel3(c,   RRT00, RRT01, RRT02);
-        float R1c  = sel3(c,   RRT01, RRT11, RRT12);
-        float R2c  = sel3(c,   RRT02, RRT12, RRT22);
-        float R0c3 = sel3(c-3, RRT00, RRT01, RRT02);
-        float R1c3 = sel3(c-3, RRT01, RRT11, RRT12);
-        float R2c3 = sel3(c-3, RRT02, RRT12, RRT22);
-        float d0  = cl3 ? q0d*R0c : 0.f;
-        float d1  = cl3 ? q0d*R1c : 0.f;
-        float dg  = cl3 ? q0d*sel3(g21,R0c,R1c,R2c) : 0.f;
-        float dg3 = c36 ? q1d*sel3(g21,R0c3,R1c3,R2c3) : 0.f;
-
-        float m0  = Pm[c]            + d0;
-        float m1  = Pm[21+c]         + d1;
-        float mr  = Pm[g21*21+c]     + dg;
-        float m3r = Pm[(3+g21)*21+c] + dg3;
-        float m6r = Pm[(6+g21)*21+c];
-        float m9  = Pm[9*21+c]  + ((c==9) ? q69 : 0.f);
-        float m10 = Pm[10*21+c] + ((c==10)? q69 : 0.f);
-        float m11 = Pm[11*21+c] + ((c==11)? q69 : 0.f);
-        float m12 = Pm[12*21+c] + ((c==12)? q24 : 0.f);
-        float m13 = Pm[13*21+c] + ((c==13)? q24 : 0.f);
-        float m14 = Pm[14*21+c] + ((c==14)? q24 : 0.f);
-
-        float Ar = (g21==0)? gdt*m1 : (g21==1)? -gdt*m0 : 0.f;
-        float bterm = Bs0*m12+Bs1*m13+Bs2*m14;
-        float e0 = mr + Bs0*m9+Bs1*m10+Bs2*m11;
-        float e1 = m3r + Ar + Cs0*m9+Cs1*m10+Cs2*m11 + bterm;
-        float e2 = m6r + hdt*Ar + dt*m3r + Ds0*m9+Ds1*m10+Ds2*m11 + hdt*bterm;
-        Eb[g21*21+c]=e0; Eb[(3+g21)*21+c]=e1; Eb[(6+g21)*21+c]=e2;
-#pragma unroll
-        for (int jj=0;jj<4;++jj){
-          int row = cw+jj;
-          float qd = (row<12)? q69 : (row<15)? q24 : q19;
-          Eb[row*21+c] = Pm[row*21+c] + ((row==c)? qd : 0.f);
-        }
+      if (n1000){
+        float Y[9];
+#pragma unroll
+        for (int k=0;k<9;++k) Y[k]=stS[21+k];
+        normalize_rot9(Y);
+        if (l>=21 && l<30){ myval = pick9(l-21,Y); stS[l] = myval; }
       }
     }
-    __syncthreads();
-
-    if (!isA){
-      const float4* h4p = (const float4*)Hds;
-      float4 h0v=h4p[0], h1v=h4p[1], h2v=h4p[2], h3v=h4p[3], h4v=h4p[4], h5v=h4p[5];
-      H0[0]=h0v.x; H0[1]=h0v.y; H0[2]=h0v.z; H0[3]=h0v.w;
-      H0[4]=h1v.x; H0[5]=h1v.y; H0[6]=h1v.z; H0[7]=h1v.w;
-      H0[8]=h2v.x; H0[9]=h2v.y; H0[10]=h2v.z; H0[11]=h2v.w;
-      H1[0]=h3v.x; H1[1]=h3v.y; H1[2]=h3v.z; H1[3]=h3v.w;
-      H1[4]=h4v.x; H1[5]=h4v.y; H1[6]=h4v.z; H1[7]=h4v.w;
-      H1[8]=h5v.x; H1[9]=h5v.y; H1[10]=h5v.z; H1[11]=h5v.w;
-
-      float p0=0.f, p1=0.f;
-      if (l<63){
-        int r = c21;
-        const float* Er = Eb + r*21;
-        float e0a=Er[0], e1a=Er[1];
-        float eg=Er[g21], e3g=Er[3+g21], e6g=Er[6+g21];
-        float e9=Er[9],e10=Er[10],e11=Er[11],e12=Er[12],e13=Er[13],e14=Er[14];
-        float Ag = (g21==0)? gdt*e1a : (g21==1)? -gdt*e0a : 0.f;
-        float bterm = Bs0*e12+Bs1*e13+Bs2*e14;
-        pnv[0] = eg + Bs0*e9+Bs1*e10+Bs2*e11;
-        pnv[1] = e3g + Ag + Cs0*e9+Cs1*e10+Cs2*e11 + bterm;
-        pnv[2] = e6g + hdt*Ag + dt*e3g + Ds0*e9+Ds1*e10+Ds2*e11 + hdt*bterm;
-        pnv[3] = Er[cw]; pnv[4] = Er[cw+1]; pnv[5] = Er[cw+2]; pnv[6] = Er[cw+3];
-
-        PnS[r*21 + g21]   = pnv[0];
-        PnS[r*21 + 3+g21] = pnv[1];
-        PnS[r*21 + 6+g21] = pnv[2];
-        PnS[r*21 + cw]    = pnv[3];
-        PnS[r*21 + cw+1]  = pnv[4];
-        PnS[r*21 + cw+2]  = pnv[5];
-        PnS[r*21 + cw+3]  = pnv[6];
-
-        float c1a = sel3(g21, H0[0], H0[1], H0[2]);
-        float c3a = sel3(g21, H0[3], 0.f,   H0[8]);
-        float c4a = sel3(g21, H0[4], 0.f,   H0[9]);
-        float c5a = sel3(g21, H0[5], H0[6], H0[10]);
-        float c6a = sel3(g21, 0.f,   H0[7], H0[11]);
-        float c1b = sel3(g21, H1[0], H1[1], H1[2]);
-        float c3b = sel3(g21, H1[3], 0.f,   H1[8]);
-        float c4b = sel3(g21, H1[4], 0.f,   H1[9]);
-        float c5b = sel3(g21, H1[5], H1[6], H1[10]);
-        float c6b = sel3(g21, 0.f,   H1[7], H1[11]);
-        p0 = c1a*pnv[1] + c3a*pnv[3] + c4a*pnv[4] + c5a*pnv[5] + c6a*pnv[6];
-        p1 = c1b*pnv[1] + c3b*pnv[3] + c4b*pnv[4] + c5b*pnv[5] + c6b*pnv[6];
-      }
-      hpr0 = p0 + __shfl(p0, l1) + __shfl(p0, l2);
-      hpr1 = p1 + __shfl(p1, l1) + __shfl(p1, l2);
-      if (l<21) HPs2[l] = make_float2(hpr0, hpr1);
-    }
-    __syncthreads();
-
-    if (isA){
-      float2 myhp = HPs2[(l<21)? l : 0];
-      float hph00=0.f, hph01=0.f, hph10=0.f, hph11=0.f;
-#pragma unroll
-      for(int k=0;k<12;++k){
-        float2 hp = HPs2[cols[k]];
-        hph00 += hp.x*H0[k]; hph01 += hp.x*H1[k];
-        hph10 += hp.y*H0[k]; hph11 += hp.y*H1[k];
-      }
-      float s00 = hph00 + crm0, s01 = hph01, s10 = hph10, s11 = hph11 + crm1;
-      float idet = 1.0f/(s00*s11 - s01*s10);
-      float i00 =  s11*idet, i01 = -s01*idet, i10 = -s10*idet, i11 = s00*idet;
-      float K0 = i00*myhp.x + i01*myhp.y;
-      float K1 = i10*myhp.x + i11*myhp.y;
-      float dxval = K0*rr0 + K1*rr1;
-
-      int db = __float_as_int(dxval);
-      float dx0 = __int_as_float(__builtin_amdgcn_readlane(db, 0));
-      float dx1 = __int_as_float(__builtin_amdgcn_readlane(db, 1));
-      float dx2 = __int_as_float(__builtin_amdgcn_readlane(db, 2));
-      float dx3 = __int_as_float(__builtin_amdgcn_readlane(db, 3));
-      float dx4 = __int_as_float(__builtin_amdgcn_readlane(db, 4));
-      float dx5 = __int_as_float(__builtin_amdgcn_readlane(db, 5));
-      float dx6 = __int_as_float(__builtin_amdgcn_readlane(db, 6));
-      float dx7 = __int_as_float(__builtin_amdgcn_readlane(db, 7));
-      float dx8 = __int_as_float(__builtin_amdgcn_readlane(db, 8));
-      float dx15 = __int_as_float(__builtin_amdgcn_readlane(db, 15));
-      float dx16 = __int_as_float(__builtin_amdgcn_readlane(db, 16));
-      float dx17 = __int_as_float(__builtin_amdgcn_readlane(db, 17));
-      int src = (l>=30 && l<33)? (l-12) : ((l>=15 && l<21)? (l-6) : 0);
-      float dxadd = __shfl(dxval, src);
-
-      float t2x = dx0*dx0+dx1*dx1+dx2*dx2;
-      float cX,k1X,k2X,j1X;
-      if (t2x < 1e-4f){
-        cX  = 1.f - t2x*(0.5f - t2x*((1.f/24.f) - t2x*(1.f/720.f)));
-        k2X = 1.f - t2x*((1.f/6.f) - t2x*((1.f/120.f) - t2x*(1.f/5040.f)));
-        k1X = 0.5f - t2x*((1.f/24.f) - t2x*(1.f/720.f));
-        j1X = (1.f/6.f) - t2x*((1.f/120.f) - t2x*(1.f/5040.f));
-      } else {
-        float a = sqrtf(t2x);
-        cX = __cosf(a);
-        float s = __sinf(a);
-        k2X = s/a; k1X = (1.f-cX)/t2x; j1X = (1.f-k2X)/t2x;
-      }
-      float dR[9];
-      dR[0]=cX+k1X*dx0*dx0;      dR[1]=k1X*dx0*dx1-k2X*dx2; dR[2]=k1X*dx0*dx2+k2X*dx1;
-      dR[3]=k1X*dx0*dx1+k2X*dx2; dR[4]=cX+k1X*dx1*dx1;      dR[5]=k1X*dx1*dx2-k2X*dx0;
-      dR[6]=k1X*dx0*dx2-k2X*dx1; dR[7]=k1X*dx1*dx2+k2X*dx0; dR[8]=cX+k1X*dx2*dx2;
-      float Jm[9];
-      Jm[0]=k2X+j1X*dx0*dx0;      Jm[1]=j1X*dx0*dx1-k1X*dx2; Jm[2]=j1X*dx0*dx2+k1X*dx1;
-      Jm[3]=j1X*dx0*dx1+k1X*dx2;  Jm[4]=k2X+j1X*dx1*dx1;     Jm[5]=j1X*dx1*dx2-k1X*dx0;
-      Jm[6]=j1X*dx0*dx2-k1X*dx1;  Jm[7]=j1X*dx1*dx2+k1X*dx0; Jm[8]=k2X+j1X*dx2*dx2;
-      float Ec[9];
-      rot_from_t2(dx15*dx15+dx16*dx16+dx17*dx17, dx15,dx16,dx17, Ec);
-
-      float myval = 0.f;
-      if (l<9){
-        int ro=(l>=6)?2:((l>=3)?1:0); int co=l-3*ro;
-        float d0=sel3(ro,dR[0],dR[3],dR[6]), d1=sel3(ro,dR[1],dR[4],dR[7]), d2=sel3(ro,dR[2],dR[5],dR[8]);
-        float n0=sel3(co,Rn[0],Rn[1],Rn[2]), n1=sel3(co,Rn[3],Rn[4],Rn[5]), n2=sel3(co,Rn[6],Rn[7],Rn[8]);
-        myval = d0*n0 + d1*n1 + d2*n2;
-      } else if (l<15){
-        int j=l-9; bool isv=(j<3); int ro = isv? j : (j-3);
-        float x0 = isv? vn0:pn0, x1 = isv? vn1:pn1, x2 = isv? vn2:pn2;
-        float y0 = isv? dx3:dx6, y1 = isv? dx4:dx7, y2 = isv? dx5:dx8;
-        float d0=sel3(ro,dR[0],dR[3],dR[6]), d1=sel3(ro,dR[1],dR[4],dR[7]), d2=sel3(ro,dR[2],dR[5],dR[8]);
-        float j0=sel3(ro,Jm[0],Jm[3],Jm[6]), j1m=sel3(ro,Jm[1],Jm[4],Jm[7]), j2m=sel3(ro,Jm[2],Jm[5],Jm[8]);
-        myval = d0*x0 + d1*x1 + d2*x2 + j0*y0 + j1m*y1 + j2m*y2;
-      } else if (l<21){
-        float old = (l<18)? sel3(l-15,bw0,bw1,bw2) : sel3(l-18,ba0,ba1,ba2);
-        myval = old + dxadd;
-      } else if (l<30){
-        int j=l-21; int ro=(j>=6)?2:((j>=3)?1:0); int co=j-3*ro;
-        float e0=sel3(ro,Ec[0],Ec[3],Ec[6]), e1=sel3(ro,Ec[1],Ec[4],Ec[7]), e2=sel3(ro,Ec[2],Ec[5],Ec[8]);
-        float r0=sel3(co,Rc[0],Rc[1],Rc[2]), r1=sel3(co,Rc[3],Rc[4],Rc[5]), r2=sel3(co,Rc[6],Rc[7],Rc[8]);
-        myval = e0*r0 + e1*r1 + e2*r2;
-      } else if (l<33){
-        myval = sel3(l-30,tc0,tc1,tc2) + dxadd;
-      }
-      if (l<33) stS[l] = myval;
-      if (l>=33 && l<36) stS[l] = sel3(l-33, tB-tA, cm0, cm1);
-
-      bool n100 = (i==nx100), n1000 = (i==nx1000);
-      if (n100) nx100 += 100;
-      if (n1000) nx1000 += 1000;
-      if (n100 || n1000){
-        WAVE_SYNC();
-        if (n100){
-          float X[9];
-#pragma unroll
-          for (int k=0;k<9;++k) X[k]=stS[k];
-          normalize_rot9(X);
-          if (l<9){ myval = pick9(l,X); stS[l] = myval; }
-        }
-        if (n1000){
-          float Y[9];
-#pragma unroll
-          for (int k=0;k<9;++k) Y[k]=stS[21+k];
-          normalize_rot9(Y);
-          if (l>=21 && l<30){ myval = pick9(l-21,Y); stS[l] = myval; }
-        }
-      }
-      if (l<33) op[i*ostr] = myval;
-    } else {
-      float hph00=0.f, hph01=0.f, hph10=0.f, hph11=0.f;
-#pragma unroll
-      for(int k=0;k<12;++k){
-        float2 hp = HPs2[cols[k]];
-        hph00 += hp.x*H0[k]; hph01 += hp.x*H1[k];
-        hph10 += hp.y*H0[k]; hph11 += hp.y*H1[k];
-      }
-      float s00 = hph00 + crm0, s01 = hph01, s10 = hph10, s11 = hph11 + crm1;
-      float idet = 1.0f/(s00*s11 - s01*s10);
-      float i00 =  s11*idet, i01 = -s01*idet, i10 = -s10*idet, i11 = s00*idet;
-      float s01q = 0.5f*(s01 + s10);
-      float K0 = i00*hpr0 + i01*hpr1;
-      float K1 = i10*hpr0 + i11*hpr1;
-
-      if (l<63){
-        int r = c21;
-#pragma unroll
-        for (int s=0;s<7;++s){
-          int j = (s<3)? (g21 + 3*s) : (cw + (s-3));
-          float pnT = PnS[j*21 + r];
-          float2 hpj = HPs2[j];
-          float kjx = i00*hpj.x + i01*hpj.y;
-          float kjy = i10*hpj.x + i11*hpj.y;
-          float base  = 0.5f*(pnv[s] + pnT);
-          float cross = (K0*hpj.x + K1*hpj.y) + (kjx*hpr0 + kjy*hpr1);
-          float quad  = (K0*kjx)*s00 + (K0*kjy + K1*kjx)*s01q + (K1*kjy)*s11;
-          Pm[r*21+j] = base - cross + quad;
-        }
-      }
-    }
-    __syncthreads();
+
+    if (l<33) op[i*ostr] = myval;
+
+    WAVE_SYNC();
   }
 }
 
@@ -522,5 +465,5 @@
   const float* v_mes = (const float*)d_in[3];
   const float* ang0  = (const float*)d_in[5];
   int N = in_sizes[0];
-  iekf_scan_kernel<<<dim3(1), dim3(128), 0, stream>>>(t, u, mcov, v_mes, ang0, (float*)d_out, N);
-}
+  iekf_scan_kernel<<<dim3(1), dim3(64), 0, stream>>>(t, u, mcov, v_mes, ang0, (float*)d_out, N);
+}
```

Measured after the change: 44.76 ms. 1.15x faster.
